# Kernel tuning notes

Measured on AMD Instinct MI355X. Metric: run time of the kernel, lower is better.

## Reference

```python
import jax, jax.numpy as jnp
import numpy as np

N_NODES = 50000
N_EDGES = 800000
EMB = 96
LAYER_NUM = 3


def setup_inputs() -> dict:
    key = jax.random.key(0)
    k1, k2, k3, k4 = jax.random.split(key, 4)
    X = jax.random.normal(k1, (N_NODES, EMB), dtype=jnp.float32)
    vals = jax.random.uniform(k2, (N_EDGES,), dtype=jnp.float32)
    rows = jax.random.randint(k3, (N_EDGES,), 0, N_NODES, dtype=jnp.int64)
    cols = jax.random.randint(k4, (N_EDGES,), 0, N_NODES, dtype=jnp.int64)
    return {"X": X, "vals": vals, "rows": rows, "cols": cols}


def reference(X, vals, rows, cols):
    # Eval-mode GNN forward: dropout layers are identity, graph is not dropped.
    # Per layer: agg = A @ ego  (COO SpMM via gather + segment_sum), then
    # ego = agg + agg * ego (elementwise gating). Output = mean over all layers.
    N = X.shape[0]
    ego = X
    acc = X  # running sum of layer embeddings (layer 0 = X)
    for _ in range(LAYER_NUM):
        # SpMM: gather source features, scale by edge values, scatter-add to rows
        msgs = vals[:, None] * ego[cols]          # [E, D]
        agg = jax.ops.segment_sum(msgs, rows, num_segments=N)  # [N, D]
        ego = agg + agg * ego
        acc = acc + ego
    return acc / jnp.asarray(LAYER_NUM + 1, dtype=X.dtype)
```

## Files before the change

kernel.cpp:

```cpp
#include <hip/hip_runtime.h>
#include <hip/hip_bf16.h>


#define N_NODES 50000
#define N_EDGES 800000
#define EMB 96
#define C16 12
#define TPR 6
#define PAD 64
#define NCHUNK (N_NODES * C16)
#define Q8U4 8

#define NBUCK 196
#define RPB 256
#define CAP 5000
#define CNT_PAD 16
#define EDGE_BLOCKS 782
#define CONV_BLOCKS ((N_NODES * TPR + 255) / 256)
#define VB_SETUP (EDGE_BLOCKS + CONV_BLOCKS)
#define VB_SPMM ((N_NODES * TPR + 255) / 256)

__device__ __forceinline__ float bflo(unsigned u) { return __uint_as_float(u << 16); }
__device__ __forceinline__ float bfhi(unsigned u) { return __uint_as_float(u & 0xffff0000u); }

__device__ __forceinline__ void unpack8(float* d, const uint4& u) {
    d[0] = bflo(u.x); d[1] = bfhi(u.x);
    d[2] = bflo(u.y); d[3] = bfhi(u.y);
    d[4] = bflo(u.z); d[5] = bfhi(u.z);
    d[6] = bflo(u.w); d[7] = bfhi(u.w);
}

__device__ __forceinline__ unsigned packbf(float a, float b) {
    unsigned ua = __float_as_uint(a);
    unsigned ub = __float_as_uint(b);
    ua = (ua + 0x7fffu + ((ua >> 16) & 1u)) >> 16;
    ub = (ub + 0x7fffu + ((ub >> 16) & 1u)) & 0xffff0000u;
    return ua | ub;
}

__device__ __forceinline__ unsigned q8w(const int* m) {
    return (unsigned)(m[0] & 255) | ((unsigned)(m[1] & 255) << 8) |
           ((unsigned)(m[2] & 255) << 16) | ((unsigned)(m[3] & 255) << 24);
}

__device__ __forceinline__ void q8enc(const float* f, uint4* mout,
                                      unsigned short* sout) {
    float mx = 0.f;
#pragma unroll
    for (int k = 0; k < 16; ++k) mx = fmaxf(mx, fabsf(f[k]));
    unsigned sb = 0;
    float inv = 0.f;
    if (mx > 1e-30f) {
        float sc = mx * (1.0078125f / 127.0f);
        unsigned u = __float_as_uint(sc);
        sb = (u + 0x7fffu + ((u >> 16) & 1u)) >> 16;
        inv = 1.0f / __uint_as_float(sb << 16);
    }
    int m[16];
#pragma unroll
    for (int k = 0; k < 16; ++k) {
        int v = __float2int_rn(f[k] * inv);
        m[k] = min(127, max(-127, v));
    }
    uint4 o;
    o.x = q8w(m); o.y = q8w(m + 4); o.z = q8w(m + 8); o.w = q8w(m + 12);
    *mout = o;
    *sout = (unsigned short)sb;
}

__device__ __forceinline__ void fma_q8x4(float* s, float c, unsigned w) {
    s[0] = fmaf(c, (float)((int)(w << 24) >> 24), s[0]);
    s[1] = fmaf(c, (float)((int)(w << 16) >> 24), s[1]);
    s[2] = fmaf(c, (float)((int)(w << 8) >> 24), s[2]);
    s[3] = fmaf(c, (float)((int)w >> 24), s[3]);
}

__device__ __forceinline__ void fma_q8x16(float* s, float c, const uint4& x) {
    fma_q8x4(s,      c, x.x);
    fma_q8x4(s + 4,  c, x.y);
    fma_q8x4(s + 8,  c, x.z);
    fma_q8x4(s + 12, c, x.w);
}


__global__ void setup_kernel(const float4* __restrict__ X4,
                             uint4* __restrict__ Xb,
                             uint4* __restrict__ Xq8,
                             const int4* __restrict__ rows4,
                             const int4* __restrict__ cols4,
                             const float4* __restrict__ vals4,
                             int* __restrict__ bucket_cnt,
                             uint2* __restrict__ bucket_buf) {
    __shared__ int hist[NBUCK];
    __shared__ int gbase[NBUCK];
    int tid = threadIdx.x;

    if (blockIdx.x < EDGE_BLOCKS) {
        for (int i = tid; i < NBUCK; i += 256) hist[i] = 0;
        __syncthreads();

        int e = blockIdx.x * 256 + tid;
        bool act = (e < N_EDGES / 4);
        int4 r, c; float4 v;
        int b0 = 0, b1 = 0, b2 = 0, b3 = 0;
        int k0 = 0, k1 = 0, k2 = 0, k3 = 0;
        if (act) {
            r = rows4[e]; c = cols4[e]; v = vals4[e];
            b0 = r.x >> 8; b1 = r.y >> 8; b2 = r.z >> 8; b3 = r.w >> 8;
            k0 = atomicAdd(&hist[b0], 1);
            k1 = atomicAdd(&hist[b1], 1);
            k2 = atomicAdd(&hist[b2], 1);
            k3 = atomicAdd(&hist[b3], 1);
        }
        __syncthreads();

        for (int i = tid; i < NBUCK; i += 256)
            gbase[i] = atomicAdd(&bucket_cnt[i * CNT_PAD], hist[i]);
        __syncthreads();

        if (act) {
            uint2 p;
            int d;
            d = gbase[b0] + k0;
            if (d < CAP) {
                p.x = (unsigned)c.x | ((unsigned)(r.x & 255) << 24);
                p.y = __float_as_uint(v.x);
                bucket_buf[b0 * CAP + d] = p;
            }
            d = gbase[b1] + k1;
            if (d < CAP) {
                p.x = (unsigned)c.y | ((unsigned)(r.y & 255) << 24);
                p.y = __float_as_uint(v.y);
                bucket_buf[b1 * CAP + d] = p;
            }
            d = gbase[b2] + k2;
            if (d < CAP) {
                p.x = (unsigned)c.z | ((unsigned)(r.z & 255) << 24);
                p.y = __float_as_uint(v.z);
                bucket_buf[b2 * CAP + d] = p;
            }
            d = gbase[b3] + k3;
            if (d < CAP) {
                p.x = (unsigned)c.w | ((unsigned)(r.w & 255) << 24);
                p.y = __float_as_uint(v.w);
                bucket_buf[b3 * CAP + d] = p;
            }
        }
    } else {
        int th = (blockIdx.x - EDGE_BLOCKS) * 256 + tid;
        if (th < N_NODES * TPR) {
            int row = th / TPR;
            int ct  = th % TPR;
            const float4* Xr = X4 + row * 24;
            float4 a = Xr[2 * ct];
            float4 b = Xr[2 * ct + 1];
            float4 c = Xr[2 * ct + 12];
            float4 d = Xr[2 * ct + 13];
            uint4 oa, ob;
            oa.x = packbf(a.x, a.y); oa.y = packbf(a.z, a.w);
            oa.z = packbf(b.x, b.y); oa.w = packbf(b.z, b.w);
            ob.x = packbf(c.x, c.y); ob.y = packbf(c.z, c.w);
            ob.z = packbf(d.x, d.y); ob.w = packbf(d.z, d.w);
            Xb[row * C16 + ct]       = oa;
            Xb[row * C16 + ct + TPR] = ob;
            float f[16] = {a.x, a.y, a.z, a.w, b.x, b.y, b.z, b.w,
                           c.x, c.y, c.z, c.w, d.x, d.y, d.z, d.w};
            unsigned short sb;
            uint4 mq;
            q8enc(f, &mq, &sb);
            Xq8[row * Q8U4 + ct] = mq;
            ((unsigned short*)Xq8)[row * 64 + 48 + ct] = sb;
        }
    }
}

__global__ void ell_build_kernel(const int* __restrict__ bucket_cnt,
                                 const uint2* __restrict__ bucket_buf,
                                 int2* __restrict__ ell,
                                 int* __restrict__ cnt) {
    __shared__ int lc[RPB];
    int b = blockIdx.x;
    int tid = threadIdx.x;
    if (tid < RPB) lc[tid] = 0;
    __syncthreads();

    int n = bucket_cnt[b * CNT_PAD];
    if (n > CAP) n = CAP;
    const uint2* buf = bucket_buf + b * CAP;
    for (int i = tid; i < n; i += 512) {
        uint2 rec = buf[i];
        int rl = rec.x >> 24;
        int slot = atomicAdd(&lc[rl], 1);
        if (slot < PAD) {
            int2 p;
            p.x = (int)(rec.x & 0x00ffffffu);
            p.y = (int)rec.y;
            ell[(b * RPB + rl) * PAD + slot] = p;
        }
    }
    __syncthreads();
    if (tid < RPB) {
        int row = b * RPB + tid;
        if (row < N_NODES) {
            int d = lc[tid];
            cnt[row] = (d > PAD) ? PAD : d;
        }
    }
}

template <int MODE>
__global__ void spmm_fused_kernel(const uint4* __restrict__ ego_in,
                                  const uint4* __restrict__ q8_in,
                                  uint4* __restrict__ ego_out,
                                  uint4* __restrict__ q8_out,
                                  const int* __restrict__ cnt,
                                  const int4* __restrict__ ell4,
                                  const uint4* __restrict__ xb,
                                  const uint4* __restrict__ e1v,
                                  float4* __restrict__ acc) {
    int tid = blockIdx.x * blockDim.x + threadIdx.x;
    if (tid >= N_NODES * TPR) return;
    int row = tid / TPR;
    int ct  = tid % TPR;

    int deg = cnt[row];
    const int4* ep = ell4 + row * (PAD / 2);
    const unsigned short* qs = (const unsigned short*)q8_in;

    float s[16] = {0.f, 0.f, 0.f, 0.f, 0.f, 0.f, 0.f, 0.f,
                   0.f, 0.f, 0.f, 0.f, 0.f, 0.f, 0.f, 0.f};

    int j = 0;
    for (; j + 4 <= deg; j += 4) {
        int4 pA = ep[j >> 1];
        int4 pB = ep[(j >> 1) + 1];
        uint4 x0 = q8_in[pA.x * Q8U4 + ct];
        uint4 x1 = q8_in[pA.z * Q8U4 + ct];
        uint4 x2 = q8_in[pB.x * Q8U4 + ct];
        uint4 x3 = q8_in[pB.z * Q8U4 + ct];
        float c0 = __int_as_float(pA.y) * bflo((unsigned)qs[pA.x * 64 + 48 + ct]);
        float c1 = __int_as_float(pA.w) * bflo((unsigned)qs[pA.z * 64 + 48 + ct]);
        float c2 = __int_as_float(pB.y) * bflo((unsigned)qs[pB.x * 64 + 48 + ct]);
        float c3 = __int_as_float(pB.w) * bflo((unsigned)qs[pB.z * 64 + 48 + ct]);
        fma_q8x16(s, c0, x0);
        fma_q8x16(s, c1, x1);
        fma_q8x16(s, c2, x2);
        fma_q8x16(s, c3, x3);
    }
    for (; j + 2 <= deg; j += 2) {
        int4 pA = ep[j >> 1];
        uint4 x0 = q8_in[pA.x * Q8U4 + ct];
        uint4 x1 = q8_in[pA.z * Q8U4 + ct];
        float c0 = __int_as_float(pA.y) * bflo((unsigned)qs[pA.x * 64 + 48 + ct]);
        float c1 = __int_as_float(pA.w) * bflo((unsigned)qs[pA.z * 64 + 48 + ct]);
        fma_q8x16(s, c0, x0);
        fma_q8x16(s, c1, x1);
    }
    if (j < deg) {
        int2 p = ((const int2*)ell4)[row * PAD + j];
        uint4 x0 = q8_in[p.x * Q8U4 + ct];
        float c0 = __int_as_float(p.y) * bflo((unsigned)qs[p.x * 64 + 48 + ct]);
        fma_q8x16(s, c0, x0);
    }

    int ib = row * C16 + ct;
    uint4 ea = ego_in[ib];
    uint4 eb = ego_in[ib + TPR];
    float e0[8], e1[8];
    unpack8(e0, ea);
    unpack8(e1, eb);
    float n0[8], n1[8];
#pragma unroll
    for (int k = 0; k < 8; ++k) {
        n0[k] = fmaf(s[k],     e0[k], s[k]);
        n1[k] = fmaf(s[8 + k], e1[k], s[8 + k]);
    }

    if (MODE == 0) {
        uint4 oa, ob;
        oa.x = packbf(n0[0], n0[1]); oa.y = packbf(n0[2], n0[3]);
        oa.z = packbf(n0[4], n0[5]); oa.w = packbf(n0[6], n0[7]);
        ob.x = packbf(n1[0], n1[1]); ob.y = packbf(n1[2], n1[3]);
        ob.z = packbf(n1[4], n1[5]); ob.w = packbf(n1[6], n1[7]);
        ego_out[ib]       = oa;
        ego_out[ib + TPR] = ob;
        float f[16] = {n0[0], n0[1], n0[2], n0[3], n0[4], n0[5], n0[6], n0[7],
                       n1[0], n1[1], n1[2], n1[3], n1[4], n1[5], n1[6], n1[7]};
        unsigned short sb;
        uint4 mq;
        q8enc(f, &mq, &sb);
        q8_out[row * Q8U4 + ct] = mq;
        ((unsigned short*)q8_out)[row * 64 + 48 + ct] = sb;
    } else {
        float x0[8], x1[8], f0[8], f1[8];
        unpack8(x0, xb[ib]);
        unpack8(x1, xb[ib + TPR]);
        unpack8(f0, e1v[ib]);
        unpack8(f1, e1v[ib + TPR]);
        int ia = row * (EMB / 4) + ct * 2;
        float4 a0, a1, a2, a3;
        a0.x = (x0[0] + f0[0] + e0[0] + n0[0]) * 0.25f;
        a0.y = (x0[1] + f0[1] + e0[1] + n0[1]) * 0.25f;
        a0.z = (x0[2] + f0[2] + e0[2] + n0[2]) * 0.25f;
        a0.w = (x0[3] + f0[3] + e0[3] + n0[3]) * 0.25f;
        a1.x = (x0[4] + f0[4] + e0[4] + n0[4]) * 0.25f;
        a1.y = (x0[5] + f0[5] + e0[5] + n0[5]) * 0.25f;
        a1.z = (x0[6] + f0[6] + e0[6] + n0[6]) * 0.25f;
        a1.w = (x0[7] + f0[7] + e0[7] + n0[7]) * 0.25f;
        a2.x = (x1[0] + f1[0] + e1[0] + n1[0]) * 0.25f;
        a2.y = (x1[1] + f1[1] + e1[1] + n1[1]) * 0.25f;
        a2.z = (x1[2] + f1[2] + e1[2] + n1[2]) * 0.25f;
        a2.w = (x1[3] + f1[3] + e1[3] + n1[3]) * 0.25f;
        a3.x = (x1[4] + f1[4] + e1[4] + n1[4]) * 0.25f;
        a3.y = (x1[5] + f1[5] + e1[5] + n1[5]) * 0.25f;
        a3.z = (x1[6] + f1[6] + e1[6] + n1[6]) * 0.25f;
        a3.w = (x1[7] + f1[7] + e1[7] + n1[7]) * 0.25f;
        acc[ia]      = a0;
        acc[ia + 1]  = a1;
        acc[ia + 12] = a2;
        acc[ia + 13] = a3;
    }
}

extern "C" void kernel_launch(void* const* d_in, const int* in_sizes, int n_in,
                              void* d_out, int out_size, void* d_ws, size_t ws_size,
                              hipStream_t stream) {
    const float* X    = (const float*)d_in[0];
    const float* vals = (const float*)d_in[1];
    const int*   rows = (const int*)d_in[2];
    const int*   cols = (const int*)d_in[3];

    const size_t nodeb_bytes = (size_t)NCHUNK * sizeof(uint4);
    const size_t q8_bytes    = (size_t)N_NODES * Q8U4 * sizeof(uint4);
    const size_t ell_bytes   = (size_t)N_NODES * PAD * sizeof(int2);
    const size_t cnt_bytes   = 204800;

    float* acc = (float*)d_out;

    char* w = (char*)d_ws;
    uint4* Xb    = (uint4*)w;  w += nodeb_bytes;
    uint4* ego_a = (uint4*)w;  w += nodeb_bytes;
    uint4* ego_b = (uint4*)w;  w += nodeb_bytes;
    int2*  ell   = (int2*)w;   w += ell_bytes;
    int*   cnt   = (int*)w;    w += cnt_bytes;
    uint4* q8a   = (uint4*)w;  w += q8_bytes;
    uint4* q8b   = (uint4*)w;  w += q8_bytes;

    uint2* bucket_buf = (uint2*)ego_a;
    int*   bucket_cnt = (int*)ego_b;

    hipMemsetAsync(bucket_cnt, 0, NBUCK * CNT_PAD * sizeof(int), stream);

    setup_kernel<<<VB_SETUP, 256, 0, stream>>>(
        (const float4*)X, Xb, q8a,
        (const int4*)rows, (const int4*)cols, (const float4*)vals,
        bucket_cnt, bucket_buf);

    ell_build_kernel<<<NBUCK, 512, 0, stream>>>(bucket_cnt, bucket_buf, ell, cnt);

    spmm_fused_kernel<0><<<VB_SPMM, 256, 0, stream>>>(
        Xb, q8a, ego_a, q8b, cnt, (const int4*)ell, nullptr, nullptr, nullptr);
    spmm_fused_kernel<0><<<VB_SPMM, 256, 0, stream>>>(
        ego_a, q8b, ego_b, q8a, cnt, (const int4*)ell, nullptr, nullptr, nullptr);
    spmm_fused_kernel<1><<<VB_SPMM, 256, 0, stream>>>(
        ego_b, q8a, nullptr, nullptr, cnt, (const int4*)ell, Xb, ego_a,
        (float4*)acc);
}
```

Before: 174.5 us.

## Sort rows by degree via histogram permutation to balance SpMM wavefronts

Builds a degree histogram in the ELL build kernel, then a new perm kernel scatters row ids into degree-sorted order. The SpMM kernels read their row through this permutation so rows of similar degree share a wavefront, cutting loop divergence. The cost is an extra kernel launch, global atomics on the histogram, and the loss of contiguous row access in the output and accumulator writes.

```diff
diff --git a/kernel.cpp b/kernel.cpp
--- a/kernel.cpp
+++ b/kernel.cpp
@@ -177,7 +177,8 @@
 __global__ void ell_build_kernel(const int* __restrict__ bucket_cnt,
                                  const uint2* __restrict__ bucket_buf,
                                  int2* __restrict__ ell,
-                                 int* __restrict__ cnt) {
+                                 int* __restrict__ cnt,
+                                 int* __restrict__ hist65) {
     __shared__ int lc[RPB];
     int b = blockIdx.x;
     int tid = threadIdx.x;
@@ -203,8 +204,32 @@
         int row = b * RPB + tid;
         if (row < N_NODES) {
             int d = lc[tid];
-            cnt[row] = (d > PAD) ? PAD : d;
-        }
+            if (d > PAD) d = PAD;
+            cnt[row] = d;
+            atomicAdd(&hist65[d * CNT_PAD], 1);
+        }
+    }
+}
+
+__global__ void perm_kernel(const int* __restrict__ cnt,
+                            const int* __restrict__ hist65,
+                            int* __restrict__ cursor65,
+                            int* __restrict__ perm) {
+    __shared__ int base[PAD + 1];
+    int tid = threadIdx.x;
+    if (tid == 0) {
+        int run = 0;
+        for (int d = 0; d <= PAD; ++d) {
+            base[d] = run;
+            run += hist65[d * CNT_PAD];
+        }
+    }
+    __syncthreads();
+    for (int r = blockIdx.x * blockDim.x + tid; r < N_NODES;
+         r += gridDim.x * blockDim.x) {
+        int d = cnt[r];
+        int slot = base[d] + atomicAdd(&cursor65[d * CNT_PAD], 1);
+        perm[slot] = r;
     }
 }
 
@@ -215,12 +240,13 @@
                                   uint4* __restrict__ q8_out,
                                   const int* __restrict__ cnt,
                                   const int4* __restrict__ ell4,
+                                  const int* __restrict__ perm,
                                   const uint4* __restrict__ xb,
                                   const uint4* __restrict__ e1v,
                                   float4* __restrict__ acc) {
     int tid = blockIdx.x * blockDim.x + threadIdx.x;
     if (tid >= N_NODES * TPR) return;
-    int row = tid / TPR;
+    int row = perm[tid / TPR];
     int ct  = tid % TPR;
 
     int deg = cnt[row];
@@ -334,6 +360,7 @@
     const size_t q8_bytes    = (size_t)N_NODES * Q8U4 * sizeof(uint4);
     const size_t ell_bytes   = (size_t)N_NODES * PAD * sizeof(int2);
     const size_t cnt_bytes   = 204800;
+    const size_t perm_bytes  = 204800;
 
     float* acc = (float*)d_out;
 
@@ -345,24 +372,33 @@
     int*   cnt   = (int*)w;    w += cnt_bytes;
     uint4* q8a   = (uint4*)w;  w += q8_bytes;
     uint4* q8b   = (uint4*)w;  w += q8_bytes;
+    int*   perm  = (int*)w;    w += perm_bytes;
 
     uint2* bucket_buf = (uint2*)ego_a;
     int*   bucket_cnt = (int*)ego_b;
-
-    hipMemsetAsync(bucket_cnt, 0, NBUCK * CNT_PAD * sizeof(int), stream);
+    int*   hist65     = bucket_cnt + NBUCK * CNT_PAD;
+    int*   cursor65   = hist65 + (PAD + 1) * CNT_PAD;
+
+    hipMemsetAsync(bucket_cnt, 0,
+                   (NBUCK + 2 * (PAD + 1)) * CNT_PAD * sizeof(int), stream);
 
     setup_kernel<<<VB_SETUP, 256, 0, stream>>>(
         (const float4*)X, Xb, q8a,
         (const int4*)rows, (const int4*)cols, (const float4*)vals,
         bucket_cnt, bucket_buf);
 
-    ell_build_kernel<<<NBUCK, 512, 0, stream>>>(bucket_cnt, bucket_buf, ell, cnt);
+    ell_build_kernel<<<NBUCK, 512, 0, stream>>>(
+        bucket_cnt, bucket_buf, ell, cnt, hist65);
+
+    perm_kernel<<<NBUCK, 256, 0, stream>>>(cnt, hist65, cursor65, perm);
 
     spmm_fused_kernel<0><<<VB_SPMM, 256, 0, stream>>>(
-        Xb, q8a, ego_a, q8b, cnt, (const int4*)ell, nullptr, nullptr, nullptr);
+        Xb, q8a, ego_a, q8b, cnt, (const int4*)ell, perm,
+        nullptr, nullptr, nullptr);
     spmm_fused_kernel<0><<<VB_SPMM, 256, 0, stream>>>(
-        ego_a, q8b, ego_b, q8a, cnt, (const int4*)ell, nullptr, nullptr, nullptr);
+        ego_a, q8b, ego_b, q8a, cnt, (const int4*)ell, perm,
+        nullptr, nullptr, nullptr);
     spmm_fused_kernel<1><<<VB_SPMM, 256, 0, stream>>>(
-        ego_b, q8a, nullptr, nullptr, cnt, (const int4*)ell, Xb, ego_a,
-        (float4*)acc);
-}
+        ego_b, q8a, nullptr, nullptr, cnt, (const int4*)ell, perm,
+        Xb, ego_a, (float4*)acc);
+}
```

Result: slower. 349.1 us (+100.1%).
